# Kernel optimization log

Hardware: AMD Instinct MI355X
Metric: run time of the kernel (lower is better)

## Reference

```python
import jax, jax.numpy as jnp
import numpy as np

B, S, D, H = 4, 1024, 1024, 16
HD = D // H
EPS = 1e-5


def layer_norm(x, scale, shift):
    mean = jnp.mean(x, axis=-1, keepdims=True)
    var = jnp.mean((x - mean) ** 2, axis=-1, keepdims=True)
    return scale * (x - mean) / jnp.sqrt(var + EPS) + shift


def gelu_tanh(x):
    c = jnp.sqrt(jnp.asarray(2.0 / jnp.pi, dtype=x.dtype))
    return 0.5 * x * (1.0 + jnp.tanh(c * (x + 0.044715 * x ** 3)))


def setup_inputs() -> dict:
    key = jax.random.key(0)
    ks = jax.random.split(key, 12)
    s = 0.02
    return {
        "x": jax.random.normal(ks[0], (B, S, D), dtype=jnp.float32),
        "attention_mask": jnp.ones((B, S), dtype=jnp.int32),
        "wq": jax.random.normal(ks[1], (D, D), dtype=jnp.float32) * s,
        "wk": jax.random.normal(ks[2], (D, D), dtype=jnp.float32) * s,
        "wv": jax.random.normal(ks[3], (D, D), dtype=jnp.float32) * s,
        "wo": jax.random.normal(ks[4], (D, D), dtype=jnp.float32) * s,
        "bo": jnp.zeros((D,), dtype=jnp.float32),
        "ln1_scale": jnp.ones((D,), dtype=jnp.float32),
        "ln1_shift": jnp.zeros((D,), dtype=jnp.float32),
        "ln2_scale": jnp.ones((D,), dtype=jnp.float32),
        "ln2_shift": jnp.zeros((D,), dtype=jnp.float32),
        "w1": jax.random.normal(ks[5], (D, 4 * D), dtype=jnp.float32) * s,
        "b1": jnp.zeros((4 * D,), dtype=jnp.float32),
        "w2": jax.random.normal(ks[6], (4 * D, D), dtype=jnp.float32) * s,
        "b2": jnp.zeros((D,), dtype=jnp.float32),
    }


def reference(x, attention_mask, wq, wk, wv, wo, bo, ln1_scale, ln1_shift,
              ln2_scale, ln2_shift, w1, b1, w2, b2):
    b, s, d = x.shape
    # --- pre-norm attention ---
    shortcut = x
    h = layer_norm(x, ln1_scale, ln1_shift)
    q = (h @ wq).reshape(b, s, H, HD).transpose(0, 2, 1, 3)  # bhsd
    k = (h @ wk).reshape(b, s, H, HD).transpose(0, 2, 1, 3)
    v = (h @ wv).reshape(b, s, H, HD).transpose(0, 2, 1, 3)
    scores = jnp.einsum('bhqd,bhkd->bhqk', q, k)
    causal = jnp.triu(jnp.ones((s, s), dtype=bool), k=1)  # True above diag -> masked
    neg_inf = jnp.asarray(-jnp.inf, dtype=scores.dtype)
    scores = jnp.where(causal, neg_inf, scores)
    pad = attention_mask[:, None, None, :].astype(bool)  # (b,1,1,k)
    scores = jnp.where(pad, scores, neg_inf)
    attn = jax.nn.softmax(scores / jnp.sqrt(jnp.asarray(HD, dtype=scores.dtype)), axis=-1)
    ctx = jnp.einsum('bhqk,bhkd->bhqd', attn, v)
    ctx = ctx.transpose(0, 2, 1, 3).reshape(b, s, d)
    x = shortcut + (ctx @ wo + bo)
    # --- pre-norm FFN ---
    shortcut = x
    h = layer_norm(x, ln2_scale, ln2_shift)
    h = gelu_tanh(h @ w1 + b1) @ w2 + b2
    return shortcut + h
```

## Files before the change

kernel.cpp:

```cpp
#include <hip/hip_runtime.h>
#include <hip/hip_bf16.h>
#include <math.h>

#define B_ 4
#define S_ 1024
#define D_ 1024
#define H_ 16
#define HD_ 64

typedef __hip_bfloat16 bf16_t;
typedef __attribute__((ext_vector_type(8))) short bf16x8;
typedef __attribute__((ext_vector_type(4))) float floatx4;

__device__ __forceinline__ float bf2f(ushort u) {
  return __uint_as_float((unsigned)u << 16);
}

__global__ __launch_bounds__(256) void prep_kernel(
    const float* __restrict__ x, const float* __restrict__ ln1s,
    const float* __restrict__ ln1b, bf16_t* __restrict__ h,
    const float* __restrict__ wq, const float* __restrict__ wk,
    const float* __restrict__ wv, const float* __restrict__ wo,
    const float* __restrict__ w1, const float* __restrict__ w2,
    bf16_t* __restrict__ wqkv_t, bf16_t* __restrict__ wo_t,
    bf16_t* __restrict__ w1_t, bf16_t* __restrict__ w2_t) {
  const int id = blockIdx.x;
  if (id < 4096) {
    const int row = id;
    float4 v = ((const float4*)(x + (size_t)row * D_))[threadIdx.x];
    float s = v.x + v.y + v.z + v.w;
    float ss = v.x * v.x + v.y * v.y + v.z * v.z + v.w * v.w;
#pragma unroll
    for (int off = 32; off > 0; off >>= 1) {
      s += __shfl_xor(s, off);
      ss += __shfl_xor(ss, off);
    }
    __shared__ float ls[4], lss[4], stats[2];
    const int wave = threadIdx.x >> 6, lane = threadIdx.x & 63;
    if (lane == 0) { ls[wave] = s; lss[wave] = ss; }
    __syncthreads();
    if (threadIdx.x == 0) {
      float t = ls[0] + ls[1] + ls[2] + ls[3];
      float tt = lss[0] + lss[1] + lss[2] + lss[3];
      float mean = t * (1.0f / D_);
      stats[0] = mean;
      stats[1] = rsqrtf(tt * (1.0f / D_) - mean * mean + 1e-5f);
    }
    __syncthreads();
    const float mean = stats[0], rstd = stats[1];
    float4 sc = ((const float4*)ln1s)[threadIdx.x];
    float4 sh = ((const float4*)ln1b)[threadIdx.x];
    bf16_t ob[4];
    ob[0] = __float2bfloat16(sc.x * (v.x - mean) * rstd + sh.x);
    ob[1] = __float2bfloat16(sc.y * (v.y - mean) * rstd + sh.y);
    ob[2] = __float2bfloat16(sc.z * (v.z - mean) * rstd + sh.z);
    ob[3] = __float2bfloat16(sc.w * (v.w - mean) * rstd + sh.w);
    *(ushort4*)(h + (size_t)row * D_ + threadIdx.x * 4) = *(ushort4*)ob;
    return;
  }
  const float* W;
  bf16_t* Wt;
  int K, N, n0, k0;
  if (id < 8192) {
    const int t = id - 4096, which = t >> 10, tile = t & 1023;
    n0 = (tile & 31) * 32;
    k0 = (tile >> 5) * 32;
    K = 1024; N = 1024;
    W = which == 0 ? wq : which == 1 ? wk : which == 2 ? wv : wo;
    Wt = which < 3 ? wqkv_t + (size_t)which * 1024 * 1024 : wo_t;
  } else if (id < 12288) {
    const int tile = id - 8192;
    n0 = (tile & 127) * 32;
    k0 = (tile >> 7) * 32;
    K = 1024; N = 4096;
    W = w1; Wt = w1_t;
  } else {
    const int tile = id - 12288;
    n0 = (tile & 31) * 32;
    k0 = (tile >> 5) * 32;
    K = 4096; N = 1024;
    W = w2; Wt = w2_t;
  }
  __shared__ float t[32][33];
  const int lx = threadIdx.x & 31, ly = threadIdx.x >> 5;
#pragma unroll
  for (int r = ly; r < 32; r += 8) t[r][lx] = W[(size_t)(k0 + r) * N + n0 + lx];
  __syncthreads();
#pragma unroll
  for (int r = ly; r < 32; r += 8)
    Wt[(size_t)(n0 + r) * K + k0 + lx] = __float2bfloat16(t[lx][r]);
}

__global__ __launch_bounds__(256) void mgemm_kernel(const bf16_t* __restrict__ A,
                                                    const bf16_t* __restrict__ Bt,
                                                    const float* __restrict__ bias,
                                                    void* __restrict__ C,
                                                    int M, int N, int K, int Kc,
                                                    int mode) {
  __shared__ bf16_t As[128 * 64];
  __shared__ bf16_t Bs[128 * 64];
  const int tid = threadIdx.x;
  const int lane = tid & 63, w = tid >> 6;
  const int m0 = blockIdx.y * 128, n0 = blockIdx.x * 128;
  const int kz0 = blockIdx.z * Kc;
  const int wm = (w >> 1) * 64, wn = (w & 1) * 64;

  floatx4 zero = {0.f, 0.f, 0.f, 0.f};
  floatx4 acc[4][4];
#pragma unroll
  for (int i = 0; i < 4; i++)
#pragma unroll
    for (int j = 0; j < 4; j++) acc[i][j] = zero;

  const int ro8 = lane >> 3;
  const int g8 = ((lane & 7) ^ ro8) * 8;
  const bf16_t* ga[4];
  const bf16_t* gb[4];
  bf16_t* la[4];
  bf16_t* lb[4];
#pragma unroll
  for (int t = 0; t < 4; t++) {
    const int c = w + 4 * t;
    ga[t] = A + (size_t)(m0 + c * 8 + ro8) * K + g8;
    gb[t] = Bt + (size_t)(n0 + c * 8 + ro8) * K + g8;
    la[t] = &As[c * 512];
    lb[t] = &Bs[c * 512];
  }

  const int fr = lane & 15, quad = lane >> 4;

  for (int k0 = kz0; k0 < kz0 + Kc; k0 += 64) {
    __syncthreads();
#pragma unroll
    for (int t = 0; t < 4; t++) {
      __builtin_amdgcn_global_load_lds(
          (const __attribute__((address_space(1))) void*)(ga[t] + k0),
          (__attribute__((address_space(3))) void*)la[t], 16, 0, 0);
      __builtin_amdgcn_global_load_lds(
          (const __attribute__((address_space(1))) void*)(gb[t] + k0),
          (__attribute__((address_space(3))) void*)lb[t], 16, 0, 0);
    }
    __syncthreads();

#pragma unroll
    for (int ks = 0; ks < 2; ks++) {
      const int sq = ((quad + 4 * ks) ^ (fr & 7)) * 8;
      bf16x8 af[4], bfr[4];
#pragma unroll
      for (int i = 0; i < 4; i++) {
        af[i] = *(const bf16x8*)&As[(wm + i * 16 + fr) * 64 + sq];
        bfr[i] = *(const bf16x8*)&Bs[(wn + i * 16 + fr) * 64 + sq];
      }
#pragma unroll
      for (int i = 0; i < 4; i++)
#pragma unroll
        for (int j = 0; j < 4; j++)
          acc[i][j] = __builtin_amdgcn_mfma_f32_16x16x32_bf16(af[i], bfr[j],
                                                              acc[i][j], 0, 0, 0);
    }
  }

  bf16_t* Pz = (mode == 4)
                   ? ((bf16_t*)C + (size_t)blockIdx.z * M * N)
                   : nullptr;
#pragma unroll
  for (int j = 0; j < 4; j++) {
    const int col = n0 + wn + j * 16 + fr;
    const float bj = bias ? bias[col] : 0.f;
#pragma unroll
    for (int i = 0; i < 4; i++) {
      const int rbase = m0 + wm + i * 16 + quad * 4;
#pragma unroll
      for (int r = 0; r < 4; r++) {
        const int row = rbase + r;
        float c = acc[i][j][r] + bj;
        if (mode == 1) {
          const float xg = c;
          const float t = 0.7978845608028654f * (xg + 0.044715f * xg * xg * xg);
          const float th = 2.0f / (1.0f + __expf(-2.0f * t)) - 1.0f;
          c = 0.5f * xg * (1.0f + th);
        }
        if (mode == 4) {
          Pz[(size_t)row * N + col] = __float2bfloat16(c);
        } else {
          ((bf16_t*)C)[(size_t)row * N + col] = __float2bfloat16(c);
        }
      }
    }
  }
}

__global__ __launch_bounds__(256) void reduce2_ln_kernel(
    const bf16_t* __restrict__ P, size_t slice, const float* __restrict__ x,
    const float* __restrict__ bias, const float* __restrict__ scale,
    const float* __restrict__ shift, float* __restrict__ out,
    bf16_t* __restrict__ h) {
  const int row = blockIdx.x;
  const size_t e = (size_t)row * D_ + threadIdx.x * 4;
  const float4 xv = *(const float4*)(x + e);
  const ushort4 p0 = *(const ushort4*)((const ushort*)P + e);
  const ushort4 p1 = *(const ushort4*)((const ushort*)P + slice + e);
  const float4 bb = *(const float4*)(bias + threadIdx.x * 4);
  float4 v;
  v.x = xv.x + bf2f(p0.x) + bf2f(p1.x) + bb.x;
  v.y = xv.y + bf2f(p0.y) + bf2f(p1.y) + bb.y;
  v.z = xv.z + bf2f(p0.z) + bf2f(p1.z) + bb.z;
  v.w = xv.w + bf2f(p0.w) + bf2f(p1.w) + bb.w;
  *(float4*)(out + e) = v;

  float s = v.x + v.y + v.z + v.w;
  float ss = v.x * v.x + v.y * v.y + v.z * v.z + v.w * v.w;
#pragma unroll
  for (int off = 32; off > 0; off >>= 1) {
    s += __shfl_xor(s, off);
    ss += __shfl_xor(ss, off);
  }
  __shared__ float ls[4], lss[4], stats[2];
  const int wave = threadIdx.x >> 6, lane = threadIdx.x & 63;
  if (lane == 0) { ls[wave] = s; lss[wave] = ss; }
  __syncthreads();
  if (threadIdx.x == 0) {
    float t = ls[0] + ls[1] + ls[2] + ls[3];
    float tt = lss[0] + lss[1] + lss[2] + lss[3];
    float mean = t * (1.0f / D_);
    stats[0] = mean;
    stats[1] = rsqrtf(tt * (1.0f / D_) - mean * mean + 1e-5f);
  }
  __syncthreads();
  const float mean = stats[0], rstd = stats[1];
  const float4 sc = *(const float4*)(scale + threadIdx.x * 4);
  const float4 sh = *(const float4*)(shift + threadIdx.x * 4);
  bf16_t ob[4];
  ob[0] = __float2bfloat16(sc.x * (v.x - mean) * rstd + sh.x);
  ob[1] = __float2bfloat16(sc.y * (v.y - mean) * rstd + sh.y);
  ob[2] = __float2bfloat16(sc.z * (v.z - mean) * rstd + sh.z);
  ob[3] = __float2bfloat16(sc.w * (v.w - mean) * rstd + sh.w);
  *(ushort4*)(h + e) = *(ushort4*)ob;
}

__global__ __launch_bounds__(256) void reduce4_kernel(const bf16_t* __restrict__ P,
                                                      size_t slice,
                                                      const float* __restrict__ bias,
                                                      float* __restrict__ out,
                                                      int N) {
  const size_t e = ((size_t)blockIdx.x * 256 + threadIdx.x) * 4;
  const ushort* Pu = (const ushort*)P;
  const ushort4 p0 = *(const ushort4*)(Pu + e);
  const ushort4 p1 = *(const ushort4*)(Pu + slice + e);
  const ushort4 p2 = *(const ushort4*)(Pu + 2 * slice + e);
  const ushort4 p3 = *(const ushort4*)(Pu + 3 * slice + e);
  const float4 r = *(const float4*)(out + e);
  const float4 bb = *(const float4*)(bias + (int)(e % N));
  float4 o;
  o.x = r.x + bb.x + bf2f(p0.x) + bf2f(p1.x) + bf2f(p2.x) + bf2f(p3.x);
  o.y = r.y + bb.y + bf2f(p0.y) + bf2f(p1.y) + bf2f(p2.y) + bf2f(p3.y);
  o.z = r.z + bb.z + bf2f(p0.z) + bf2f(p1.z) + bf2f(p2.z) + bf2f(p3.z);
  o.w = r.w + bb.w + bf2f(p0.w) + bf2f(p1.w) + bf2f(p2.w) + bf2f(p3.w);
  *(float4*)(out + e) = o;
}

__global__ __launch_bounds__(256) void fattn_kernel(const bf16_t* __restrict__ QKV,
                                                    const int* __restrict__ mask,
                                                    bf16_t* __restrict__ O) {
  const int qt = gridDim.x - 1 - blockIdx.x;
  const int h = blockIdx.y, b = blockIdx.z;
  const int tid = threadIdx.x;
  const int lane = tid & 63, w = tid >> 6;
  const int tx = lane & 15, quad = lane >> 4;
  const int q0 = qt * 64;

  __shared__ ushort Ks[64 * 72];
  __shared__ ushort Vt[64 * 72];
  __shared__ ushort Ps[64 * 72];

  const ushort* qkv = (const ushort*)QKV;
  const size_t rowb = (size_t)b * S_ * 3072;
  const int koff = D_ + h * HD_, voff = 2 * D_ + h * HD_;

  bf16x8 qf[2];
#pragma unroll
  for (int ks = 0; ks < 2; ks++)
    qf[ks] = *(const bf16x8*)(qkv + rowb +
        (size_t)(q0 + w * 16 + tx) * 3072 + h * HD_ + ks * 32 + quad * 8);

  const short oneb = 0x3F80;
  bf16x8 vones = {oneb, oneb, oneb, oneb, oneb, oneb, oneb, oneb};

  floatx4 ctx[4], lacc;
#pragma unroll
  for (int nt = 0; nt < 4; nt++) {
    ctx[nt].x = 0.f; ctx[nt].y = 0.f; ctx[nt].z = 0.f; ctx[nt].w = 0.f;
  }
  lacc.x = 0.f; lacc.y = 0.f; lacc.z = 0.f; lacc.w = 0.f;

  for (int kt = 0; kt <= qt; kt++) {
    const int k0 = kt * 64;
    __syncthreads();
#pragma unroll
    for (int i = 0; i < 2; i++) {
      const int e = tid + i * 256;
      const int r = e >> 3, ch = (e & 7) * 8;
      *(uint4*)&Ks[r * 72 + ch] =
          *(const uint4*)(qkv + rowb + (size_t)(k0 + r) * 3072 + koff + ch);
    }
#pragma unroll
    for (int i = 0; i < 2; i++) {
      const int r = tid & 63;
      const int c8 = (tid >> 6) * 8 + i * 32;
      uint4 u = *(const uint4*)(qkv + rowb + (size_t)(k0 + r) * 3072 + voff + c8);
      const ushort* sv = (const ushort*)&u;
#pragma unroll
      for (int j = 0; j < 8; j++) Vt[(c8 + j) * 72 + r] = sv[j];
    }
    __syncthreads();

    floatx4 accS[4];
#pragma unroll
    for (int nt = 0; nt < 4; nt++) {
      accS[nt].x = 0.f; accS[nt].y = 0.f; accS[nt].z = 0.f; accS[nt].w = 0.f;
    }
#pragma unroll
    for (int ks = 0; ks < 2; ks++) {
      bf16x8 kf[4];
#pragma unroll
      for (int nt = 0; nt < 4; nt++)
        kf[nt] = *(const bf16x8*)&Ks[(nt * 16 + tx) * 72 + ks * 32 + quad * 8];
#pragma unroll
      for (int nt = 0; nt < 4; nt++)
        accS[nt] = __builtin_amdgcn_mfma_f32_16x16x32_bf16(qf[ks], kf[nt],
                                                           accS[nt], 0, 0, 0);
    }

#pragma unroll
    for (int nt = 0; nt < 4; nt++) {
      const int jc = k0 + nt * 16 + tx;
      const bool ok = mask[b * S_ + jc] != 0;
#pragma unroll
      for (int r = 0; r < 4; r++) {
        const int qrow = q0 + w * 16 + quad * 4 + r;
        float p = exp2f(accS[nt][r] * 0.1803368801111244f);
        if (jc > qrow || !ok) p = 0.f;
        Ps[(w * 16 + quad * 4 + r) * 72 + nt * 16 + tx] =
            ((__hip_bfloat16_raw)__float2bfloat16(p)).x;
      }
    }

#pragma unroll
    for (int ks = 0; ks < 2; ks++) {
      const bf16x8 pf = *(const bf16x8*)&Ps[(w * 16 + tx) * 72 + ks * 32 + quad * 8];
      bf16x8 vf[4];
#pragma unroll
      for (int nt = 0; nt < 4; nt++)
        vf[nt] = *(const bf16x8*)&Vt[(nt * 16 + tx) * 72 + ks * 32 + quad * 8];
#pragma unroll
      for (int nt = 0; nt < 4; nt++)
        ctx[nt] = __builtin_amdgcn_mfma_f32_16x16x32_bf16(pf, vf[nt],
                                                          ctx[nt], 0, 0, 0);
      lacc = __builtin_amdgcn_mfma_f32_16x16x32_bf16(pf, vones, lacc, 0, 0, 0);
    }
  }

  const size_t obase = (size_t)b * S_ * D_ + (size_t)h * HD_;
  float rinv[4];
#pragma unroll
  for (int r = 0; r < 4; r++) rinv[r] = 1.0f / lacc[r];
#pragma unroll
  for (int nt = 0; nt < 4; nt++)
#pragma unroll
    for (int r = 0; r < 4; r++) {
      const int q = q0 + w * 16 + quad * 4 + r;
      O[obase + (size_t)q * D_ + nt * 16 + tx] =
          __float2bfloat16(ctx[nt][r] * rinv[r]);
    }
}

extern "C" void kernel_launch(void* const* d_in, const int* in_sizes, int n_in,
                              void* d_out, int out_size, void* d_ws, size_t ws_size,
                              hipStream_t stream) {
  const float* x = (const float*)d_in[0];
  const int* mask = (const int*)d_in[1];
  const float* wq = (const float*)d_in[2];
  const float* wk = (const float*)d_in[3];
  const float* wv = (const float*)d_in[4];
  const float* wo = (const float*)d_in[5];
  const float* bo = (const float*)d_in[6];
  const float* ln2s = (const float*)d_in[9];
  const float* ln2b = (const float*)d_in[10];
  const float* w1 = (const float*)d_in[11];
  const float* b1 = (const float*)d_in[12];
  const float* w2 = (const float*)d_in[13];
  const float* b2 = (const float*)d_in[14];
  float* out = (float*)d_out;

  const int M = B_ * S_;
  char* ws = (char*)d_ws;
  const size_t MB = (size_t)1 << 20;
  bf16_t* qkv = (bf16_t*)(ws);
  bf16_t* ffn1 = (bf16_t*)(ws);
  bf16_t* ctx = (bf16_t*)(ws + 32 * MB);
  bf16_t* h = (bf16_t*)(ws + 40 * MB);
  bf16_t* wqkv_t = (bf16_t*)(ws + 48 * MB);
  bf16_t* wo_t = (bf16_t*)(ws + 54 * MB);
  bf16_t* w1_t = (bf16_t*)(ws + 56 * MB);
  bf16_t* w2_t = (bf16_t*)(ws + 64 * MB);
  bf16_t* Pa = (bf16_t*)(ws);
  bf16_t* Pf = (bf16_t*)(ws + 32 * MB);
  const size_t slice = (size_t)M * D_;

  prep_kernel<<<dim3(16384), 256, 0, stream>>>(x, (const float*)d_in[7],
                                               (const float*)d_in[8], h, wq, wk,
                                               wv, wo, w1, w2, wqkv_t, wo_t,
                                               w1_t, w2_t);

  mgemm_kernel<<<dim3(3 * D_ / 128, M / 128), 256, 0, stream>>>(
      h, wqkv_t, nullptr, qkv, M, 3 * D_, D_, D_, 0);

  fattn_kernel<<<dim3(S_ / 64, H_, B_), 256, 0, stream>>>(qkv, mask, ctx);

  mgemm_kernel<<<dim3(D_ / 128, M / 128, 2), 256, 0, stream>>>(
      ctx, wo_t, nullptr, Pa, M, D_, D_, D_ / 2, 4);

  reduce2_ln_kernel<<<dim3(M), 256, 0, stream>>>(Pa, slice, x, bo, ln2s, ln2b,
                                                 out, h);

  mgemm_kernel<<<dim3(4 * D_ / 128, M / 128), 256, 0, stream>>>(
      h, w1_t, b1, ffn1, M, 4 * D_, D_, D_, 1);

  mgemm_kernel<<<dim3(D_ / 128, M / 128, 4), 256, 0, stream>>>(
      ffn1, w2_t, nullptr, Pf, M, D_, 4 * D_, D_, 4);

  reduce4_kernel<<<dim3((size_t)M * D_ / 1024), 256, 0, stream>>>(
      Pf, slice, b2, out, D_);
}
```

Before: 383.1 us.

## Remap GEMM tiles to XCDs so each die shares A/B panels in L2

Launches each GEMM as a flat 1D grid and decodes the block index so that blocks dispatched round-robin to the same XCD (flat & 7) cover a contiguous rectangular sub-grid of output tiles. Each XCD's private L2 then holds fewer distinct A row panels and B column panels, which is meant to cut redundant HBM/L2 misses across dies. The per-GEMM partition parameters (Mt, Nt, PM) are hand-chosen to fit each shape. This relies on the hardware dispatching workgroups round-robin across the 8 XCDs, and a wrong mapping would leave tiles uncovered.

```diff
diff --git a/kernel.cpp b/kernel.cpp
--- a/kernel.cpp
+++ b/kernel.cpp
@@ -96,13 +96,23 @@
                                                     const float* __restrict__ bias,
                                                     void* __restrict__ C,
                                                     int M, int N, int K, int Kc,
+                                                    int Mt, int Nt, int PM,
                                                     int mode) {
   __shared__ bf16_t As[128 * 64];
   __shared__ bf16_t Bs[128 * 64];
   const int tid = threadIdx.x;
   const int lane = tid & 63, w = tid >> 6;
-  const int m0 = blockIdx.y * 128, n0 = blockIdx.x * 128;
-  const int kz0 = blockIdx.z * Kc;
+
+  const int flat = blockIdx.x;
+  const int xcd = flat & 7;
+  int t0 = flat >> 3;
+  const int mb = xcd % PM, nb = xcd / PM;
+  const int mt = mb * Mt + (t0 % Mt);
+  t0 /= Mt;
+  const int nt = nb * Nt + (t0 % Nt);
+  const int z = t0 / Nt;
+  const int m0 = mt * 128, n0 = nt * 128;
+  const int kz0 = z * Kc;
   const int wm = (w >> 1) * 64, wn = (w & 1) * 64;
 
   floatx4 zero = {0.f, 0.f, 0.f, 0.f};
@@ -160,9 +170,7 @@
     }
   }
 
-  bf16_t* Pz = (mode == 4)
-                   ? ((bf16_t*)C + (size_t)blockIdx.z * M * N)
-                   : nullptr;
+  bf16_t* Pz = (mode == 4) ? ((bf16_t*)C + (size_t)z * M * N) : nullptr;
 #pragma unroll
   for (int j = 0; j < 4; j++) {
     const int col = n0 + wn + j * 16 + fr;
@@ -412,22 +420,22 @@
                                                wv, wo, w1, w2, wqkv_t, wo_t,
                                                w1_t, w2_t);
 
-  mgemm_kernel<<<dim3(3 * D_ / 128, M / 128), 256, 0, stream>>>(
-      h, wqkv_t, nullptr, qkv, M, 3 * D_, D_, D_, 0);
+  mgemm_kernel<<<dim3(24 * 32), 256, 0, stream>>>(
+      h, wqkv_t, nullptr, qkv, M, 3 * D_, D_, D_, 8, 12, 4, 0);
 
   fattn_kernel<<<dim3(S_ / 64, H_, B_), 256, 0, stream>>>(qkv, mask, ctx);
 
-  mgemm_kernel<<<dim3(D_ / 128, M / 128, 2), 256, 0, stream>>>(
-      ctx, wo_t, nullptr, Pa, M, D_, D_, D_ / 2, 4);
+  mgemm_kernel<<<dim3(8 * 32 * 2), 256, 0, stream>>>(
+      ctx, wo_t, nullptr, Pa, M, D_, D_, D_ / 2, 4, 8, 8, 4);
 
   reduce2_ln_kernel<<<dim3(M), 256, 0, stream>>>(Pa, slice, x, bo, ln2s, ln2b,
                                                  out, h);
 
-  mgemm_kernel<<<dim3(4 * D_ / 128, M / 128), 256, 0, stream>>>(
-      h, w1_t, b1, ffn1, M, 4 * D_, D_, D_, 1);
-
-  mgemm_kernel<<<dim3(D_ / 128, M / 128, 4), 256, 0, stream>>>(
-      ffn1, w2_t, nullptr, Pf, M, D_, 4 * D_, D_, 4);
+  mgemm_kernel<<<dim3(32 * 32), 256, 0, stream>>>(
+      h, w1_t, b1, ffn1, M, 4 * D_, D_, D_, 16, 8, 2, 1);
+
+  mgemm_kernel<<<dim3(8 * 32 * 4), 256, 0, stream>>>(
+      ffn1, w2_t, nullptr, Pf, M, D_, 4 * D_, D_, 8, 4, 4, 4);
 
   reduce4_kernel<<<dim3((size_t)M * D_ / 1024), 256, 0, stream>>>(
       Pf, slice, b2, out, D_);
```

New measurement: 375.9 us. Within noise of the previous version (-1.9%).
